# Kernel tuning notes

Measured on AMD Instinct MI355X. Metric: run time of the kernel, lower is better.

Reference implementation:

```python
import jax, jax.numpy as jnp
import numpy as np

B, T, F, N = 262144, 3, 17, 8
EMBD = 32
DT = 0.2  # 25/5*0.04
EPS = 1e-8  # torch.cosine_similarity eps


def _mono(x, wi, bi, wo, bo):
    # monotonic_fun with increasing=False: relu(-Linear(x)) -> Linear
    h = jax.nn.relu(-(x @ wi.T + bi))  # (..., EMBD)
    return h @ wo.T + bo               # (..., 1)


def _cos(a, b):
    dot = jnp.sum(a * b, axis=-1)
    na = jnp.maximum(jnp.linalg.norm(a, axis=-1), EPS)
    nb = jnp.maximum(jnp.linalg.norm(b, axis=-1), EPS)
    return dot / (na * nb)


def _angle_clamp(vec, e, ang):
    # vec: (B,K,2), e: (B,2) -> keep forces within effective angle cone, sum over K
    keep = jnp.abs(_cos(e[:, None, :], vec)) > ang
    return jnp.sum(vec * keep[..., None], axis=1)


def setup_inputs() -> dict:
    key = jax.random.key(0)
    ks = jax.random.split(key, 8)
    ego = jax.random.normal(ks[0], (B, T, F), jnp.float32)
    ego = ego.at[:, :, 2:4].multiply(10.0)  # position scale
    nei = jax.random.normal(ks[1], (B, N, F), jnp.float32)
    nei = nei.at[:, :, 2:4].multiply(10.0).at[:, :, 4:6].multiply(0.1)
    border = jax.random.normal(ks[2], (4,), jnp.float32)
    attr_dest_para = jax.random.uniform(ks[3], (2,), jnp.float32) + 0.1  # relu(rand), keep away from 0 divisor
    eff_angle = jax.nn.sigmoid(jax.random.uniform(ks[4], (1,), jnp.float32))

    def mlp(k):
        k1, k2, k3, k4 = jax.random.split(k, 4)
        wi = jax.random.uniform(k1, (EMBD, 1), jnp.float32)      # clamped >= 0
        bi = jax.random.normal(k2, (EMBD,), jnp.float32) * 0.1
        wo = jax.random.uniform(k3, (1, EMBD), jnp.float32) * 0.1  # clamped >= 0
        bo = jax.random.normal(k4, (1,), jnp.float32) * 0.1
        return wi, bi, wo, bo

    an = mlp(ks[5])
    rn = mlp(ks[6])
    rb = mlp(ks[7])
    dl = mlp(jax.random.fold_in(key, 99))
    return dict(
        ego=ego, nei=nei, border=border,
        attr_dest_para=attr_dest_para, eff_angle=eff_angle,
        an_wi=an[0], an_bi=an[1], an_wo=an[2], an_bo=an[3],
        rn_wi=rn[0], rn_bi=rn[1], rn_wo=rn[2], rn_bo=rn[3],
        rb_wi=rb[0], rb_bi=rb[1], rb_wo=rb[2], rb_bo=rb[3],
        dl_wi=dl[0], dl_bi=dl[1], dl_wo=dl[2], dl_bo=dl[3],
    )


def reference(ego, nei, border, attr_dest_para, eff_angle,
              an_wi, an_bi, an_wo, an_bo,
              rn_wi, rn_bi, rn_wo, rn_bo,
              rb_wi, rb_bi, rb_wo, rb_bo,
              dl_wi, dl_bi, dl_wo, dl_bo):
    ego_last = ego[:, -1]  # (B,F)

    # --- attr_destination (desired_velocity=None branch) ---
    v34 = ego_last[:, 3:5]
    dv = jnp.stack([jnp.linalg.norm(v34, axis=-1),
                    jnp.zeros(ego.shape[0], ego.dtype)], axis=1)  # (B,2)
    f_dest = ((attr_dest_para[1] * dv - v34) / attr_dest_para[0])[:, None, :]  # (B,1,2)

    # --- attr_repu_neighbors ---
    r = nei[:, :, 2:4] - ego_last[:, None, 2:4]  # (B,N,2)
    mask = nei[:, :, 2:4] == 0                    # (B,N,2)
    r_norm = jnp.linalg.norm(r, axis=-1, keepdims=True)  # (B,N,1)

    # neighbor durality: quirky use of batch element 1, shared across batch
    ids_last = ego[1, -1, 8:-1]  # (8,) neighbor-id columns
    dur = jnp.zeros(N, ego.dtype)
    for t in range(ego.shape[1]):
        dur = dur + jnp.isin(ids_last, ego[1, t, 8:-1]).astype(ego.dtype)

    f_attr = _mono(r_norm, an_wi, an_bi, an_wo, an_bo) * r / r_norm \
             * _mono(dur[:, None], dl_wi, dl_bi, dl_wo, dl_bo)  # (B,N,2)*(N,1)
    f_attr = jnp.where(mask, 0.0, f_attr)

    v_nei = nei[:, :, 4:6]
    b = r_norm \
        + jnp.sum((r + v_nei * DT) ** 2, axis=-1, keepdims=True) \
        - jnp.sum((v_nei * DT) ** 2, axis=-1, keepdims=True)
    b = jnp.sqrt(b) / 2
    f_repu = _mono(b, rn_wi, rn_bi, rn_wo, rn_bo) * r / r_norm
    f_repu = jnp.where(mask, 0.0, f_repu)

    # --- repu_borders (select_lane = [0, -1]) ---
    rb_all = ego_last[:, 3, None] - border        # (B,4)
    rbv = jnp.stack([rb_all[:, 0], rb_all[:, -1]], axis=1)  # (B,2)
    rbn = jnp.abs(rbv)
    f_bor = _mono(rbn[..., None], rb_wi, rb_bi, rb_wo, rb_bo) * (rbv / rbn)[..., None]  # (B,2,1)
    f_bor = jnp.concatenate([jnp.zeros_like(f_bor), f_bor], axis=-1)  # (B,2,2): [0, fy]

    # --- angle clamp + integrate ---
    e = ego_last[:, 4:6]
    e = e / jnp.linalg.norm(e, axis=1, keepdims=True)
    a = (_angle_clamp(f_dest, e, eff_angle)
         + _angle_clamp(f_attr, e, eff_angle) + _angle_clamp(f_repu, e, eff_angle)
         + _angle_clamp(f_bor, e, eff_angle))
    v = ego_last[:, 2:4] + a * DT
    s = ego_last[:, :2] + v * DT
    return jnp.concatenate([s, v, a], axis=1)  # (B,6)
```

## Files before the change

kernel.cpp:

```cpp
#include <hip/hip_runtime.h>

#define DTC 0.2f
#define EPSC 1e-8f

__device__ __forceinline__ float mono_eval(const float* __restrict__ kn, float x) {
    int i = (kn[15] <= x) ? 16 : 0;
    i += (kn[i + 7] <= x) ? 8 : 0;
    i += (kn[i + 3] <= x) ? 4 : 0;
    i += (kn[i + 1] <= x) ? 2 : 0;
    i += (kn[i] <= x) ? 1 : 0;
    return -fmaf(kn[32 + i], x, kn[65 + i]);
}

__global__ __launch_bounds__(256) void sfm_fused(
    const float* __restrict__ ego, const float* __restrict__ nei,
    const float* __restrict__ border, const float* __restrict__ adp,
    const float* __restrict__ eang,
    const float* __restrict__ an_wi, const float* __restrict__ an_bi,
    const float* __restrict__ an_wo, const float* __restrict__ an_bo,
    const float* __restrict__ rn_wi, const float* __restrict__ rn_bi,
    const float* __restrict__ rn_wo, const float* __restrict__ rn_bo,
    const float* __restrict__ rb_wi, const float* __restrict__ rb_bi,
    const float* __restrict__ rb_wo, const float* __restrict__ rb_bo,
    const float* __restrict__ dl_wi, const float* __restrict__ dl_bi,
    const float* __restrict__ dl_wo, const float* __restrict__ dl_bo,
    float* __restrict__ out, int Bn)
{
    __shared__ float sw[360];
    __shared__ float tk[96], w1[96], w2[96], sk[96], s1[96], s2[96];

    int t = threadIdx.x;
    int l = t & 7;
    long long row = (long long)blockIdx.x * 32 + (t >> 3);
    long long prow = (row < Bn) ? row : (long long)(Bn - 1);

    const float* nr = nei + prow * 136 + l * 17 + 2;
    float nx = nr[0], ny = nr[1], vx = nr[2], vy = nr[3];
    float egv = 0.f;
    if (l < 6) egv = ego[prow * 51 + 34 + l];

    if (t < 96) {
        int f = t >> 5, k = t & 31;
        const float* wip = (f == 0) ? an_wi : ((f == 1) ? rn_wi : rb_wi);
        const float* bip = (f == 0) ? an_bi : ((f == 1) ? rn_bi : rb_bi);
        const float* wop = (f == 0) ? an_wo : ((f == 1) ? rn_wo : rb_wo);
        float wi = wip[k], bi = bip[k], wo = wop[k];
        tk[t] = -bi / wi;
        w1[t] = wi * wo;
        w2[t] = wo * bi;
    }
    if (t >= 96 && t < 104) {
        int j = t - 96;
        const float* base = ego + 51;
        float idv = base[2 * 17 + 8 + j];
        float dur = 0.f;
        for (int tt = 0; tt < 3; ++tt) {
            bool fo = false;
            for (int m = 0; m < 8; ++m) fo = fo || (idv == base[tt * 17 + 8 + m]);
            dur += fo ? 1.f : 0.f;
        }
        float acc = 0.f;
#pragma unroll
        for (int k = 0; k < 32; ++k)
            acc = fmaf(dl_wo[k], fmaxf(0.f, -fmaf(dl_wi[k], dur, dl_bi[k])), acc);
        sw[j] = acc + dl_bo[0];
    }
    if (t == 104) sw[352] = an_bo[0];
    if (t == 105) sw[353] = rn_bo[0];
    if (t == 106) sw[354] = rb_bo[0];
    if (t == 107) sw[355] = adp[0];
    if (t == 108) sw[356] = adp[1];
    if (t == 109) sw[357] = eang[0];
    if (t == 110) sw[358] = border[0];
    if (t == 111) sw[359] = border[3];
    __syncthreads();

    if (t < 96) {
        int k = t & 31, b = t & ~31;
        float my = tk[t];
        int rank = 0;
#pragma unroll
        for (int m = 0; m < 32; ++m) {
            float o = tk[b + m];
            rank += (o < my || (o == my && m < k)) ? 1 : 0;
        }
        sk[b + rank] = my;
        s1[b + rank] = w1[t];
        s2[b + rank] = w2[t];
    }
    __syncthreads();

    if (t < 96) {
        int f = t >> 5, p = t & 31, b = t & ~31;
        float sw_ = 0.f, sb_ = 0.f;
#pragma unroll
        for (int m = 0; m < 32; ++m) {
            float a = s1[b + m], c = s2[b + m];
            if (m >= p) { sw_ += a; sb_ += c; }
        }
        int base = 16 + f * 112;
        sw[base + p]      = sk[b + p];
        sw[base + 32 + p] = sw_;
        sw[base + 65 + p] = sb_;
        if (p == 0) { sw[base + 64] = 0.f; sw[base + 97] = 0.f; }
    }
    __syncthreads();

    if (row < Bn) {
        int lb = (t & 63) & ~7;
        float g0 = __shfl(egv, lb + 0, 64);
        float g1 = __shfl(egv, lb + 1, 64);
        float g2 = __shfl(egv, lb + 2, 64);
        float g3 = __shfl(egv, lb + 3, 64);
        float g4 = __shfl(egv, lb + 4, 64);
        float g5 = __shfl(egv, lb + 5, 64);

        float Rx = nx - g2, Ry = ny - g3;
        float rr = sqrtf(Rx * Rx + Ry * Ry);
        float ax = fmaf(vx, DTC, Rx), ay = fmaf(vy, DTC, Ry);
        float wx = vx * DTC, wy = vy * DTC;
        float bb = sqrtf(rr + ax * ax + ay * ay - wx * wx - wy * wy) * 0.5f;

        float an_bo_v = sw[352], rn_bo_v = sw[353], rb_bo_v = sw[354];
        float p0 = sw[355], p1 = sw[356], ang = sw[357];
        float rb0 = g3 - sw[358], rb1 = g3 - sw[359];
        float rbn0 = fabsf(rb0), rbn1 = fabsf(rb1);

        float fA = mono_eval(sw + 16, rr) + an_bo_v;
        float fR = mono_eval(sw + 128, bb) + rn_bo_v;
        float xb = (l == 1) ? rbn1 : rbn0;
        float vB = 0.f;
        if (l < 2) vB = mono_eval(sw + 240, xb) + rb_bo_v;
        float vB0 = __shfl(vB, lb + 0, 64);
        float vB1 = __shfl(vB, lb + 1, 64);

        float elen = sqrtf(g4 * g4 + g5 * g5);
        float ex = g4 / elen, ey = g5 / elen;
        float na = fmaxf(sqrtf(ex * ex + ey * ey), EPSC);

        float axs = 0.f, ays = 0.f;
#define CLAMP_ADD(VX, VY)                                                   \
        {                                                                   \
            float _vx = (VX), _vy = (VY);                                   \
            float _nv = fmaxf(sqrtf(_vx * _vx + _vy * _vy), EPSC);          \
            float _c = (ex * _vx + ey * _vy) / (na * _nv);                  \
            if (fabsf(_c) > ang) { axs += _vx; ays += _vy; }                \
        }

        float mfx = (nx == 0.f) ? 0.f : 1.f;
        float mfy = (ny == 0.f) ? 0.f : 1.f;

        {
            float coef = fA / rr * sw[l];
            CLAMP_ADD(coef * Rx * mfx, coef * Ry * mfy);
        }
        {
            float coef = fR / rr;
            CLAMP_ADD(coef * Rx * mfx, coef * Ry * mfy);
        }

#pragma unroll
        for (int m = 1; m < 8; m <<= 1) {
            axs += __shfl_xor(axs, m, 64);
            ays += __shfl_xor(ays, m, 64);
        }

        if (l == 0) {
            float dvn = sqrtf(g3 * g3 + g4 * g4);
            CLAMP_ADD((p1 * dvn - g3) / p0, -g4 / p0);
            CLAMP_ADD(0.f, vB0 * (rb0 / rbn0));
            CLAMP_ADD(0.f, vB1 * (rb1 / rbn1));

            float vxo = fmaf(axs, DTC, g2);
            float vyo = fmaf(ays, DTC, g3);
            float* op = out + row * 6;
            op[0] = fmaf(vxo, DTC, g0);
            op[1] = fmaf(vyo, DTC, g1);
            op[2] = vxo; op[3] = vyo;
            op[4] = axs; op[5] = ays;
        }
#undef CLAMP_ADD
    }
}

extern "C" void kernel_launch(void* const* d_in, const int* in_sizes, int n_in,
                              void* d_out, int out_size, void* d_ws, size_t ws_size,
                              hipStream_t stream) {
    const float* ego    = (const float*)d_in[0];
    const float* nei    = (const float*)d_in[1];
    const float* border = (const float*)d_in[2];
    const float* adp    = (const float*)d_in[3];
    const float* eang   = (const float*)d_in[4];
    const float* an_wi  = (const float*)d_in[5];
    const float* an_bi  = (const float*)d_in[6];
    const float* an_wo  = (const float*)d_in[7];
    const float* an_bo  = (const float*)d_in[8];
    const float* rn_wi  = (const float*)d_in[9];
    const float* rn_bi  = (const float*)d_in[10];
    const float* rn_wo  = (const float*)d_in[11];
    const float* rn_bo  = (const float*)d_in[12];
    const float* rb_wi  = (const float*)d_in[13];
    const float* rb_bi  = (const float*)d_in[14];
    const float* rb_wo  = (const float*)d_in[15];
    const float* rb_bo  = (const float*)d_in[16];
    const float* dl_wi  = (const float*)d_in[17];
    const float* dl_bi  = (const float*)d_in[18];
    const float* dl_wo  = (const float*)d_in[19];
    const float* dl_bo  = (const float*)d_in[20];
    float* out = (float*)d_out;
    (void)d_ws; (void)ws_size;

    int Bn = in_sizes[0] / (3 * 17);
    int grid = (Bn + 31) / 32;
    sfm_fused<<<grid, 256, 0, stream>>>(ego, nei, border, adp, eang,
                                        an_wi, an_bi, an_wo, an_bo,
                                        rn_wi, rn_bi, rn_wo, rn_bo,
                                        rb_wi, rb_bi, rb_wo, rb_bo,
                                        dl_wi, dl_bi, dl_wo, dl_bo,
                                        out, Bn);
}
```

Before: 285.8 us.

## Use persistent grid-stride blocks with software-prefetched next-group loads

The launch now uses at most 2048 blocks, and each block loops over groups of 32 rows in grid-stride fashion, so the per-block weight preprocessing (sorting, prefix sums, duration MLP) is paid once per block instead of once per 32 rows. Inside the loop the nei and ego values for the next group are loaded before the current group is computed, to hide global memory latency. Each lane now reads all six ego values directly instead of receiving them by shuffle. The cost is more live registers and fewer blocks to spread latency across.

```diff
diff --git a/kernel.cpp b/kernel.cpp
--- a/kernel.cpp
+++ b/kernel.cpp
@@ -24,20 +24,12 @@
     const float* __restrict__ rb_wo, const float* __restrict__ rb_bo,
     const float* __restrict__ dl_wi, const float* __restrict__ dl_bi,
     const float* __restrict__ dl_wo, const float* __restrict__ dl_bo,
-    float* __restrict__ out, int Bn)
+    float* __restrict__ out, int Bn, int nGroups)
 {
     __shared__ float sw[360];
     __shared__ float tk[96], w1[96], w2[96], sk[96], s1[96], s2[96];
 
     int t = threadIdx.x;
-    int l = t & 7;
-    long long row = (long long)blockIdx.x * 32 + (t >> 3);
-    long long prow = (row < Bn) ? row : (long long)(Bn - 1);
-
-    const float* nr = nei + prow * 136 + l * 17 + 2;
-    float nx = nr[0], ny = nr[1], vx = nr[2], vy = nr[3];
-    float egv = 0.f;
-    if (l < 6) egv = ego[prow * 51 + 34 + l];
 
     if (t < 96) {
         int f = t >> 5, k = t & 31;
@@ -106,80 +98,113 @@
     }
     __syncthreads();
 
-    if (row < Bn) {
-        int lb = (t & 63) & ~7;
-        float g0 = __shfl(egv, lb + 0, 64);
-        float g1 = __shfl(egv, lb + 1, 64);
-        float g2 = __shfl(egv, lb + 2, 64);
-        float g3 = __shfl(egv, lb + 3, 64);
-        float g4 = __shfl(egv, lb + 4, 64);
-        float g5 = __shfl(egv, lb + 5, 64);
-
-        float Rx = nx - g2, Ry = ny - g3;
-        float rr = sqrtf(Rx * Rx + Ry * Ry);
-        float ax = fmaf(vx, DTC, Rx), ay = fmaf(vy, DTC, Ry);
-        float wx = vx * DTC, wy = vy * DTC;
-        float bb = sqrtf(rr + ax * ax + ay * ay - wx * wx - wy * wy) * 0.5f;
-
-        float an_bo_v = sw[352], rn_bo_v = sw[353], rb_bo_v = sw[354];
-        float p0 = sw[355], p1 = sw[356], ang = sw[357];
-        float rb0 = g3 - sw[358], rb1 = g3 - sw[359];
-        float rbn0 = fabsf(rb0), rbn1 = fabsf(rb1);
-
-        float fA = mono_eval(sw + 16, rr) + an_bo_v;
-        float fR = mono_eval(sw + 128, bb) + rn_bo_v;
-        float xb = (l == 1) ? rbn1 : rbn0;
-        float vB = 0.f;
-        if (l < 2) vB = mono_eval(sw + 240, xb) + rb_bo_v;
-        float vB0 = __shfl(vB, lb + 0, 64);
-        float vB1 = __shfl(vB, lb + 1, 64);
-
-        float elen = sqrtf(g4 * g4 + g5 * g5);
-        float ex = g4 / elen, ey = g5 / elen;
-        float na = fmaxf(sqrtf(ex * ex + ey * ey), EPSC);
-
-        float axs = 0.f, ays = 0.f;
+    const int l = t & 7;
+    const int sub = t >> 3;
+    const int lb = (t & 63) & ~7;
+
+    const float an_bo_v = sw[352], rn_bo_v = sw[353], rb_bo_v = sw[354];
+    const float p0 = sw[355], p1 = sw[356], ang = sw[357];
+    const float bor0 = sw[358], bor3 = sw[359];
+    const float dlf = sw[l];
+
+    long long grp = blockIdx.x;
+    const long long gstride = gridDim.x;
+    if (grp >= nGroups) return;
+
+    float nx, ny, vx, vy, g0, g1, g2, g3, g4, g5;
+    {
+        long long row = grp * 32 + sub;
+        long long prow = (row < Bn) ? row : (long long)(Bn - 1);
+        const float* nr = nei + prow * 136 + l * 17 + 2;
+        nx = nr[0]; ny = nr[1]; vx = nr[2]; vy = nr[3];
+        const float* er = ego + prow * 51 + 34;
+        g0 = er[0]; g1 = er[1]; g2 = er[2]; g3 = er[3]; g4 = er[4]; g5 = er[5];
+    }
+
+    for (;;) {
+        const long long ngrp = grp + gstride;
+        const bool more = (ngrp < nGroups);
+        float nx2, ny2, vx2, vy2, h0, h1, h2, h3, h4, h5;
+        {
+            long long row = more ? (ngrp * 32 + sub) : 0;
+            long long prow = (row < Bn) ? row : (long long)(Bn - 1);
+            const float* nr = nei + prow * 136 + l * 17 + 2;
+            nx2 = nr[0]; ny2 = nr[1]; vx2 = nr[2]; vy2 = nr[3];
+            const float* er = ego + prow * 51 + 34;
+            h0 = er[0]; h1 = er[1]; h2 = er[2]; h3 = er[3]; h4 = er[4]; h5 = er[5];
+        }
+
+        long long row = grp * 32 + sub;
+        if (row < Bn) {
+            float Rx = nx - g2, Ry = ny - g3;
+            float rr = sqrtf(Rx * Rx + Ry * Ry);
+            float axq = fmaf(vx, DTC, Rx), ayq = fmaf(vy, DTC, Ry);
+            float wxq = vx * DTC, wyq = vy * DTC;
+            float bb = sqrtf(rr + axq * axq + ayq * ayq - wxq * wxq - wyq * wyq) * 0.5f;
+
+            float rb0 = g3 - bor0, rb1 = g3 - bor3;
+            float rbn0 = fabsf(rb0), rbn1 = fabsf(rb1);
+
+            float fA = mono_eval(sw + 16, rr) + an_bo_v;
+            float fR = mono_eval(sw + 128, bb) + rn_bo_v;
+            float xb = (l == 1) ? rbn1 : rbn0;
+            float vB = 0.f;
+            if (l < 2) vB = mono_eval(sw + 240, xb) + rb_bo_v;
+            float vB0 = __shfl(vB, lb + 0, 64);
+            float vB1 = __shfl(vB, lb + 1, 64);
+
+            float elen = sqrtf(g4 * g4 + g5 * g5);
+            float ex = g4 / elen, ey = g5 / elen;
+            float na = fmaxf(sqrtf(ex * ex + ey * ey), EPSC);
+
+            float axs = 0.f, ays = 0.f;
 #define CLAMP_ADD(VX, VY)                                                   \
-        {                                                                   \
-            float _vx = (VX), _vy = (VY);                                   \
-            float _nv = fmaxf(sqrtf(_vx * _vx + _vy * _vy), EPSC);          \
-            float _c = (ex * _vx + ey * _vy) / (na * _nv);                  \
-            if (fabsf(_c) > ang) { axs += _vx; ays += _vy; }                \
-        }
-
-        float mfx = (nx == 0.f) ? 0.f : 1.f;
-        float mfy = (ny == 0.f) ? 0.f : 1.f;
-
-        {
-            float coef = fA / rr * sw[l];
-            CLAMP_ADD(coef * Rx * mfx, coef * Ry * mfy);
-        }
-        {
-            float coef = fR / rr;
-            CLAMP_ADD(coef * Rx * mfx, coef * Ry * mfy);
-        }
-
-#pragma unroll
-        for (int m = 1; m < 8; m <<= 1) {
-            axs += __shfl_xor(axs, m, 64);
-            ays += __shfl_xor(ays, m, 64);
-        }
-
-        if (l == 0) {
-            float dvn = sqrtf(g3 * g3 + g4 * g4);
-            CLAMP_ADD((p1 * dvn - g3) / p0, -g4 / p0);
-            CLAMP_ADD(0.f, vB0 * (rb0 / rbn0));
-            CLAMP_ADD(0.f, vB1 * (rb1 / rbn1));
-
-            float vxo = fmaf(axs, DTC, g2);
-            float vyo = fmaf(ays, DTC, g3);
-            float* op = out + row * 6;
-            op[0] = fmaf(vxo, DTC, g0);
-            op[1] = fmaf(vyo, DTC, g1);
-            op[2] = vxo; op[3] = vyo;
-            op[4] = axs; op[5] = ays;
-        }
+            {                                                               \
+                float _vx = (VX), _vy = (VY);                               \
+                float _nv = fmaxf(sqrtf(_vx * _vx + _vy * _vy), EPSC);      \
+                float _c = (ex * _vx + ey * _vy) / (na * _nv);              \
+                if (fabsf(_c) > ang) { axs += _vx; ays += _vy; }            \
+            }
+
+            float mfx = (nx == 0.f) ? 0.f : 1.f;
+            float mfy = (ny == 0.f) ? 0.f : 1.f;
+
+            {
+                float coef = fA / rr * dlf;
+                CLAMP_ADD(coef * Rx * mfx, coef * Ry * mfy);
+            }
+            {
+                float coef = fR / rr;
+                CLAMP_ADD(coef * Rx * mfx, coef * Ry * mfy);
+            }
+
+#pragma unroll
+            for (int m = 1; m < 8; m <<= 1) {
+                axs += __shfl_xor(axs, m, 64);
+                ays += __shfl_xor(ays, m, 64);
+            }
+
+            if (l == 0) {
+                float dvn = sqrtf(g3 * g3 + g4 * g4);
+                CLAMP_ADD((p1 * dvn - g3) / p0, -g4 / p0);
+                CLAMP_ADD(0.f, vB0 * (rb0 / rbn0));
+                CLAMP_ADD(0.f, vB1 * (rb1 / rbn1));
+
+                float vxo = fmaf(axs, DTC, g2);
+                float vyo = fmaf(ays, DTC, g3);
+                float* op = out + row * 6;
+                op[0] = fmaf(vxo, DTC, g0);
+                op[1] = fmaf(vyo, DTC, g1);
+                op[2] = vxo; op[3] = vyo;
+                op[4] = axs; op[5] = ays;
+            }
 #undef CLAMP_ADD
+        }
+
+        if (!more) break;
+        grp = ngrp;
+        nx = nx2; ny = ny2; vx = vx2; vy = vy2;
+        g0 = h0; g1 = h1; g2 = h2; g3 = h3; g4 = h4; g5 = h5;
     }
 }
 
@@ -211,11 +236,12 @@
     (void)d_ws; (void)ws_size;
 
     int Bn = in_sizes[0] / (3 * 17);
-    int grid = (Bn + 31) / 32;
+    int nGroups = (Bn + 31) / 32;
+    int grid = (nGroups < 2048) ? nGroups : 2048;
     sfm_fused<<<grid, 256, 0, stream>>>(ego, nei, border, adp, eang,
                                         an_wi, an_bi, an_wo, an_bo,
                                         rn_wi, rn_bi, rn_wo, rn_bo,
                                         rb_wi, rb_bi, rb_wo, rb_bo,
                                         dl_wi, dl_bi, dl_wo, dl_bo,
-                                        out, Bn);
+                                        out, Bn, nGroups);
 }
```

After: 282.4 us. Within noise of the previous version (-1.2%).

## Map one batch row per thread with vectorized neighbor loads

Applied to the files above, without the earlier changes.

Changes the thread mapping from eight lanes per row (one per neighbor) to one thread per row that loops over all eight neighbors, loading only the needed float4 chunks of the neighbor record. This removes the cross-lane shuffles and reductions, and cuts the per-block weight-table setup (sort and prefix sums) by a factor of eight since each block now covers 256 rows. The trade-offs are strided, uncoalesced per-thread loads across 544-byte records, higher register pressure, an approximate reciprocal in place of division, and copysign in place of rb/|rb|, which gives ±1 rather than NaN when rb is zero.

```diff
diff --git a/kernel.cpp b/kernel.cpp
--- a/kernel.cpp
+++ b/kernel.cpp
@@ -29,15 +29,21 @@
     __shared__ float sw[360];
     __shared__ float tk[96], w1[96], w2[96], sk[96], s1[96], s2[96];
 
-    int t = threadIdx.x;
-    int l = t & 7;
-    long long row = (long long)blockIdx.x * 32 + (t >> 3);
-    long long prow = (row < Bn) ? row : (long long)(Bn - 1);
-
-    const float* nr = nei + prow * 136 + l * 17 + 2;
-    float nx = nr[0], ny = nr[1], vx = nr[2], vy = nr[3];
-    float egv = 0.f;
-    if (l < 6) egv = ego[prow * 51 + 34 + l];
+    const int t = threadIdx.x;
+    const int row = blockIdx.x * 256 + t;
+    const int prow = (row < Bn) ? row : (Bn - 1);
+
+    const float4* nq = (const float4*)(nei + (size_t)prow * 136);
+    float4 a0 = nq[0],  b0 = nq[1];
+    float4 a1 = nq[4],  b1 = nq[5];
+    float4 a2 = nq[9];
+    float4 a3 = nq[13], b3 = nq[14];
+    float4 a4 = nq[17], b4 = nq[18];
+    float4 a5 = nq[21], b5 = nq[22];
+    float4 a6 = nq[26];
+    float4 a7 = nq[30], b7 = nq[31];
+    const float* er = ego + (size_t)prow * 51 + 34;
+    float g0 = er[0], g1 = er[1], g2 = er[2], g3 = er[3], g4 = er[4], g5 = er[5];
 
     if (t < 96) {
         int f = t >> 5, k = t & 31;
@@ -107,32 +113,10 @@
     __syncthreads();
 
     if (row < Bn) {
-        int lb = (t & 63) & ~7;
-        float g0 = __shfl(egv, lb + 0, 64);
-        float g1 = __shfl(egv, lb + 1, 64);
-        float g2 = __shfl(egv, lb + 2, 64);
-        float g3 = __shfl(egv, lb + 3, 64);
-        float g4 = __shfl(egv, lb + 4, 64);
-        float g5 = __shfl(egv, lb + 5, 64);
-
-        float Rx = nx - g2, Ry = ny - g3;
-        float rr = sqrtf(Rx * Rx + Ry * Ry);
-        float ax = fmaf(vx, DTC, Rx), ay = fmaf(vy, DTC, Ry);
-        float wx = vx * DTC, wy = vy * DTC;
-        float bb = sqrtf(rr + ax * ax + ay * ay - wx * wx - wy * wy) * 0.5f;
-
-        float an_bo_v = sw[352], rn_bo_v = sw[353], rb_bo_v = sw[354];
-        float p0 = sw[355], p1 = sw[356], ang = sw[357];
+        const float an_bo_v = sw[352], rn_bo_v = sw[353], rb_bo_v = sw[354];
+        const float p0 = sw[355], p1 = sw[356], ang = sw[357];
         float rb0 = g3 - sw[358], rb1 = g3 - sw[359];
         float rbn0 = fabsf(rb0), rbn1 = fabsf(rb1);
-
-        float fA = mono_eval(sw + 16, rr) + an_bo_v;
-        float fR = mono_eval(sw + 128, bb) + rn_bo_v;
-        float xb = (l == 1) ? rbn1 : rbn0;
-        float vB = 0.f;
-        if (l < 2) vB = mono_eval(sw + 240, xb) + rb_bo_v;
-        float vB0 = __shfl(vB, lb + 0, 64);
-        float vB1 = __shfl(vB, lb + 1, 64);
 
         float elen = sqrtf(g4 * g4 + g5 * g5);
         float ex = g4 / elen, ey = g5 / elen;
@@ -147,39 +131,51 @@
             if (fabsf(_c) > ang) { axs += _vx; ays += _vy; }                \
         }
 
-        float mfx = (nx == 0.f) ? 0.f : 1.f;
-        float mfy = (ny == 0.f) ? 0.f : 1.f;
-
-        {
-            float coef = fA / rr * sw[l];
-            CLAMP_ADD(coef * Rx * mfx, coef * Ry * mfy);
-        }
-        {
-            float coef = fR / rr;
-            CLAMP_ADD(coef * Rx * mfx, coef * Ry * mfy);
-        }
-
-#pragma unroll
-        for (int m = 1; m < 8; m <<= 1) {
-            axs += __shfl_xor(axs, m, 64);
-            ays += __shfl_xor(ays, m, 64);
-        }
-
-        if (l == 0) {
-            float dvn = sqrtf(g3 * g3 + g4 * g4);
-            CLAMP_ADD((p1 * dvn - g3) / p0, -g4 / p0);
-            CLAMP_ADD(0.f, vB0 * (rb0 / rbn0));
-            CLAMP_ADD(0.f, vB1 * (rb1 / rbn1));
-
-            float vxo = fmaf(axs, DTC, g2);
-            float vyo = fmaf(ays, DTC, g3);
-            float* op = out + row * 6;
-            op[0] = fmaf(vxo, DTC, g0);
-            op[1] = fmaf(vyo, DTC, g1);
-            op[2] = vxo; op[3] = vyo;
-            op[4] = axs; op[5] = ays;
-        }
+#define DO_REC(L, NX, NY, VX, VY)                                           \
+        {                                                                   \
+            float nx = (NX), ny = (NY), vx = (VX), vy = (VY);               \
+            float Rx = nx - g2, Ry = ny - g3;                               \
+            float rr = sqrtf(Rx * Rx + Ry * Ry);                            \
+            float axq = fmaf(vx, DTC, Rx), ayq = fmaf(vy, DTC, Ry);         \
+            float wxq = vx * DTC, wyq = vy * DTC;                           \
+            float bb = sqrtf(rr + axq * axq + ayq * ayq                     \
+                             - wxq * wxq - wyq * wyq) * 0.5f;               \
+            float fA = mono_eval(sw + 16, rr) + an_bo_v;                    \
+            float fR = mono_eval(sw + 128, bb) + rn_bo_v;                   \
+            float inv_rr = __builtin_amdgcn_rcpf(rr);                       \
+            float mfx = (nx == 0.f) ? 0.f : 1.f;                            \
+            float mfy = (ny == 0.f) ? 0.f : 1.f;                            \
+            float coefA = fA * inv_rr * sw[L];                              \
+            CLAMP_ADD(coefA * Rx * mfx, coefA * Ry * mfy);                  \
+            float coefR = fR * inv_rr;                                      \
+            CLAMP_ADD(coefR * Rx * mfx, coefR * Ry * mfy);                  \
+        }
+
+        DO_REC(0, a0.z, a0.w, b0.x, b0.y);
+        DO_REC(1, a1.w, b1.x, b1.y, b1.z);
+        DO_REC(2, a2.x, a2.y, a2.z, a2.w);
+        DO_REC(3, a3.y, a3.z, a3.w, b3.x);
+        DO_REC(4, a4.z, a4.w, b4.x, b4.y);
+        DO_REC(5, a5.w, b5.x, b5.y, b5.z);
+        DO_REC(6, a6.x, a6.y, a6.z, a6.w);
+        DO_REC(7, a7.y, a7.z, a7.w, b7.x);
+#undef DO_REC
+
+        float dvn = sqrtf(g3 * g3 + g4 * g4);
+        CLAMP_ADD((p1 * dvn - g3) / p0, -g4 / p0);
+        float vB0 = mono_eval(sw + 240, rbn0) + rb_bo_v;
+        float vB1 = mono_eval(sw + 240, rbn1) + rb_bo_v;
+        CLAMP_ADD(0.f, vB0 * copysignf(1.f, rb0));
+        CLAMP_ADD(0.f, vB1 * copysignf(1.f, rb1));
 #undef CLAMP_ADD
+
+        float vxo = fmaf(axs, DTC, g2);
+        float vyo = fmaf(ays, DTC, g3);
+        float2* op = (float2*)(out + (size_t)row * 6);
+        float2 o0; o0.x = fmaf(vxo, DTC, g0); o0.y = fmaf(vyo, DTC, g1);
+        float2 o1; o1.x = vxo; o1.y = vyo;
+        float2 o2; o2.x = axs; o2.y = ays;
+        op[0] = o0; op[1] = o1; op[2] = o2;
     }
 }
 
@@ -211,7 +207,7 @@
     (void)d_ws; (void)ws_size;
 
     int Bn = in_sizes[0] / (3 * 17);
-    int grid = (Bn + 31) / 32;
+    int grid = (Bn + 255) / 256;
     sfm_fused<<<grid, 256, 0, stream>>>(ego, nei, border, adp, eang,
                                         an_wi, an_bi, an_wo, an_bo,
                                         rn_wi, rn_bi, rn_wo, rn_bo,
```

Result: faster. 278.7 us (-2.5%).
